# Optimization experiments

Measured on AMD Instinct MI355X. Metric: run time of the kernel, lower is better.

The kernel has to match this reference:

```python
import jax, jax.numpy as jnp
import numpy as np

B, T, I, H, OUT, L = 256, 1200, 16, 128, 1, 2


def _lstm_layer(x, W_ih, W_hh, b_ih, b_hh):
    # x: [B, T, Din]; W_ih: [4H, Din]; W_hh: [4H, H]
    # Precompute input contribution for all timesteps (one big GEMM),
    # then scan only the recurrent part.
    pre = jnp.einsum('btd,gd->btg', x, W_ih) + b_ih + b_hh  # [B, T, 4H]
    pre = jnp.swapaxes(pre, 0, 1)  # [T, B, 4H]
    h0 = jnp.zeros((x.shape[0], W_hh.shape[1]), dtype=x.dtype)
    c0 = jnp.zeros_like(h0)

    def step(carry, p_t):
        h, c = carry
        g = p_t + h @ W_hh.T  # [B, 4H]
        i, f, gg, o = jnp.split(g, 4, axis=-1)  # torch gate order: i, f, g, o
        i = jax.nn.sigmoid(i)
        f = jax.nn.sigmoid(f)
        gg = jnp.tanh(gg)
        o = jax.nn.sigmoid(o)
        c = f * c + i * gg
        h = o * jnp.tanh(c)
        return (h, c), h

    (_, _), hs = jax.lax.scan(step, (h0, c0), pre)  # hs: [T, B, H]
    return jnp.swapaxes(hs, 0, 1)  # [B, T, H]


def setup_inputs() -> dict:
    key = jax.random.key(0)
    ks = jax.random.split(key, 12)
    s = 0.08  # small init scale to keep gates unsaturated
    inp = {
        'x': jax.random.normal(ks[0], (B, T, I), dtype=jnp.float32),
        'W_ih0': jax.random.normal(ks[1], (4 * H, I), dtype=jnp.float32) * s,
        'W_hh0': jax.random.normal(ks[2], (4 * H, H), dtype=jnp.float32) * s,
        'b_ih0': jax.random.normal(ks[3], (4 * H,), dtype=jnp.float32) * s,
        'b_hh0': jax.random.normal(ks[4], (4 * H,), dtype=jnp.float32) * s,
        'W_ih1': jax.random.normal(ks[5], (4 * H, H), dtype=jnp.float32) * s,
        'W_hh1': jax.random.normal(ks[6], (4 * H, H), dtype=jnp.float32) * s,
        'b_ih1': jax.random.normal(ks[7], (4 * H,), dtype=jnp.float32) * s,
        'b_hh1': jax.random.normal(ks[8], (4 * H,), dtype=jnp.float32) * s,
        'W_lin': jax.random.normal(ks[9], (OUT, H), dtype=jnp.float32) * s,
        'b_lin': jax.random.normal(ks[10], (OUT,), dtype=jnp.float32) * s,
    }
    return inp


def reference(x, W_ih0, W_hh0, b_ih0, b_hh0, W_ih1, W_hh1, b_ih1, b_hh1, W_lin, b_lin):
    h1 = _lstm_layer(x, W_ih0, W_hh0, b_ih0, b_hh0)   # [B, T, H]
    h2 = _lstm_layer(h1, W_ih1, W_hh1, b_ih1, b_hh1)  # [B, T, H]
    out = jax.nn.relu(h2)
    out = jnp.einsum('bth,oh->bto', out, W_lin) + b_lin  # [B, T, OUT]
    return out.reshape(-1, 12)  # [B*T*OUT/12, 12]
```

## Files before the change

kernel.cpp:

```cpp
#include <hip/hip_runtime.h>
#include <hip/hip_fp16.h>

#define B_ 256
#define T_ 1200
#define I_ 16
#define H_ 128

typedef __attribute__((ext_vector_type(2))) _Float16 h2;
typedef __attribute__((ext_vector_type(8))) _Float16 f16x8;

union f16x8u { f16x8 v; h2 h[4]; _Float16 s[8]; };

#if __has_builtin(__builtin_amdgcn_fdot2)
__device__ __forceinline__ float fdot2(h2 a, h2 b, float c) {
  return __builtin_amdgcn_fdot2(a, b, c, false);
}
#else
__device__ __forceinline__ float fdot2(h2 a, h2 b, float c) {
  return fmaf((float)a.x, (float)b.x, fmaf((float)a.y, (float)b.y, c));
}
#endif

template <int PAT>
__device__ __forceinline__ float qbcast(float x) {
  return __int_as_float(__builtin_amdgcn_update_dpp(0, __float_as_int(x), PAT, 0xF, 0xF, true));
}

__device__ __forceinline__ float wred(float x) {
  x += __int_as_float(__builtin_amdgcn_update_dpp(0, __float_as_int(x), 0x141, 0xF, 0xF, true));
  x += __int_as_float(__builtin_amdgcn_update_dpp(0, __float_as_int(x), 0x140, 0xF, 0xF, true));
  x += __shfl_xor(x, 16);
  x += __shfl_xor(x, 32);
  return x;
}

__device__ __forceinline__ float tanh_(float x) {
  return 1.f - 2.f * __builtin_amdgcn_rcpf(1.f + __expf(2.f * x));
}

__device__ __forceinline__ void load_row_h2(const float* __restrict__ p, h2* w) {
#pragma unroll
  for (int i = 0; i < 32; ++i) {
    const float4 v = *(const float4*)(p + 4 * i);
    w[2 * i].x     = (_Float16)v.x; w[2 * i].y     = (_Float16)v.y;
    w[2 * i + 1].x = (_Float16)v.z; w[2 * i + 1].y = (_Float16)v.w;
  }
}

__device__ __forceinline__ void lds_barrier() {
  __builtin_amdgcn_sched_barrier(0);
  asm volatile("s_waitcnt lgkmcnt(0)" ::: "memory");
  __builtin_amdgcn_s_barrier();
  __builtin_amdgcn_sched_barrier(0);
}

__global__ __launch_bounds__(512, 2) void lstm_one(
    const float* __restrict__ xin,
    const float* __restrict__ Wih0, const float* __restrict__ Whh0,
    const float* __restrict__ bih0, const float* __restrict__ bhh0,
    const float* __restrict__ Wih1, const float* __restrict__ Whh1,
    const float* __restrict__ bih1, const float* __restrict__ bhh1,
    const float* __restrict__ Wlin, const float* __restrict__ blin,
    float* __restrict__ out)
{
  __shared__ __align__(16) __half xs[T_ * I_];
  __shared__ __align__(16) __half h0b[2][H_];
  __shared__ __align__(16) __half h1b[2][H_];
  __shared__ __align__(16) float red[2][8];

  const int tid = threadIdx.x;
  const int q = tid & 3;
  const int j = tid >> 2;
  const int g = q * H_ + j;
  const int b = blockIdx.x;

  {
    const float4* xg4 = (const float4*)(xin + (size_t)b * T_ * I_);
    for (int idx = tid; idx < T_ * I_ / 4; idx += 512) {
      const float4 v = xg4[idx];
      xs[4 * idx]     = __float2half(v.x);
      xs[4 * idx + 1] = __float2half(v.y);
      xs[4 * idx + 2] = __float2half(v.z);
      xs[4 * idx + 3] = __float2half(v.w);
    }
  }

  h2 w0[64], wi[64], w1[64], wx[8];
  load_row_h2(Whh0 + (size_t)g * H_, w0);
  load_row_h2(Wih1 + (size_t)g * H_, wi);
  load_row_h2(Whh1 + (size_t)g * H_, w1);
  {
    const float* px = Wih0 + (size_t)g * I_;
#pragma unroll
    for (int i = 0; i < 4; ++i) {
      const float4 v = *(const float4*)(px + 4 * i);
      wx[2 * i].x     = (_Float16)v.x; wx[2 * i].y     = (_Float16)v.y;
      wx[2 * i + 1].x = (_Float16)v.z; wx[2 * i + 1].y = (_Float16)v.w;
    }
  }
  const float bs0 = bih0[g] + bhh0[g];
  const float bs1 = bih1[g] + bhh1[g];
  const float wl = Wlin[j];
  const float bl = blin[0];
  const float s0 = (q == 2) ? 1.f : 0.f;
  const float s1 = (q == 2) ? -2.f : 1.f;
  const float s2 = (q == 2) ? 2.f : -1.f;

  if (tid < H_) {
    h0b[0][tid] = __float2half(0.f);
    h1b[0][tid] = __float2half(0.f);
    h1b[1][tid] = __float2half(0.f);
  }
  float cst0 = 0.f, cst1 = 0.f, hv1p = 0.f;
  float* op = out + (size_t)b * T_;
  __syncthreads();

#pragma unroll 1
  for (int u = 0; u <= T_ + 2; ++u) {
    const int rb = u & 1, nb = rb ^ 1;

    if (u >= 2 && u <= T_ + 1) {
      const float val = wred(fmaxf(hv1p, 0.f) * wl);
      if ((tid & 63) == 0) red[rb][tid >> 6] = val;
    }
    if (u >= 3) {
      const int m = u - 3;
      if (tid == ((m & 7) << 6)) {
        const float4 r0 = *(const float4*)(&red[nb][0]);
        const float4 r1 = *(const float4*)(&red[nb][4]);
        op[m] = bl + r0.x + r0.y + r0.z + r0.w + r1.x + r1.y + r1.z + r1.w;
      }
    }

    float A0 = 0.f, A1 = 0.f, A2 = 0.f, A3 = 0.f;
    float B0 = 0.f, B1 = 0.f, B2 = 0.f, B3 = 0.f;
    float C0 = 0.f, C1 = 0.f, C2 = 0.f, C3 = 0.f;

    if (u >= 1 && u < T_) {
#pragma unroll
      for (int i = 0; i < 16; ++i) {
        f16x8u u8; u8.v = *(const f16x8*)(&h0b[rb][8 * i]);
        A0 = fdot2(w0[4 * i],     u8.h[0], A0);
        A1 = fdot2(w0[4 * i + 1], u8.h[1], A1);
        A2 = fdot2(w0[4 * i + 2], u8.h[2], A2);
        A3 = fdot2(w0[4 * i + 3], u8.h[3], A3);
        B0 = fdot2(wi[4 * i],     u8.h[0], B0);
        B1 = fdot2(wi[4 * i + 1], u8.h[1], B1);
        B2 = fdot2(wi[4 * i + 2], u8.h[2], B2);
        B3 = fdot2(wi[4 * i + 3], u8.h[3], B3);
      }
    } else if (u == T_) {
#pragma unroll
      for (int i = 0; i < 16; ++i) {
        f16x8u u8; u8.v = *(const f16x8*)(&h0b[rb][8 * i]);
        B0 = fdot2(wi[4 * i],     u8.h[0], B0);
        B1 = fdot2(wi[4 * i + 1], u8.h[1], B1);
        B2 = fdot2(wi[4 * i + 2], u8.h[2], B2);
        B3 = fdot2(wi[4 * i + 3], u8.h[3], B3);
      }
    }

    if (u < T_) {
#pragma unroll
      for (int m2 = 0; m2 < 2; ++m2) {
        f16x8u u8; u8.v = *(const f16x8*)(&xs[u * I_ + 8 * m2]);
        A0 = fdot2(wx[4 * m2],     u8.h[0], A0);
        A1 = fdot2(wx[4 * m2 + 1], u8.h[1], A1);
        A2 = fdot2(wx[4 * m2 + 2], u8.h[2], A2);
        A3 = fdot2(wx[4 * m2 + 3], u8.h[3], A3);
      }
      const float pre = (A0 + A1) + (A2 + A3) + bs0;
      const float act = fmaf(s1, __builtin_amdgcn_rcpf(1.f + __expf(s2 * pre)), s0);
      const float ig = qbcast<0x00>(act);
      const float fg = qbcast<0x55>(act);
      const float gg = qbcast<0xAA>(act);
      const float og = qbcast<0xFF>(act);
      cst0 = fg * cst0 + ig * gg;
      const float hv0 = og * tanh_(cst0);
      if (q == 0) h0b[nb][j] = __float2half(hv0);
    }

    if (u >= 1 && u <= T_) {
#pragma unroll
      for (int i = 0; i < 16; ++i) {
        f16x8u u8; u8.v = *(const f16x8*)(&h1b[rb][8 * i]);
        C0 = fdot2(w1[4 * i],     u8.h[0], C0);
        C1 = fdot2(w1[4 * i + 1], u8.h[1], C1);
        C2 = fdot2(w1[4 * i + 2], u8.h[2], C2);
        C3 = fdot2(w1[4 * i + 3], u8.h[3], C3);
      }
      const float pre = (B0 + B1) + (B2 + B3) + (C0 + C1) + (C2 + C3) + bs1;
      const float act = fmaf(s1, __builtin_amdgcn_rcpf(1.f + __expf(s2 * pre)), s0);
      const float ig = qbcast<0x00>(act);
      const float fg = qbcast<0x55>(act);
      const float gg = qbcast<0xAA>(act);
      const float og = qbcast<0xFF>(act);
      cst1 = fg * cst1 + ig * gg;
      hv1p = og * tanh_(cst1);
      if (q == 0) h1b[nb][j] = __float2half(hv1p);
    }

    if (u <= T_ + 1) lds_barrier();
  }
}

extern "C" void kernel_launch(void* const* d_in, const int* in_sizes, int n_in,
                              void* d_out, int out_size, void* d_ws, size_t ws_size,
                              hipStream_t stream) {
  lstm_one<<<B_, 512, 0, stream>>>(
      (const float*)d_in[0],
      (const float*)d_in[1], (const float*)d_in[2],
      (const float*)d_in[3], (const float*)d_in[4],
      (const float*)d_in[5], (const float*)d_in[6],
      (const float*)d_in[7], (const float*)d_in[8],
      (const float*)d_in[9], (const float*)d_in[10],
      (float*)d_out);
}
```

Baseline: 1.933 ms.

## Split each LSTM unit's dot products across 8 lanes with DPP reductions

The block grows from 512 to 1024 threads. Each group of 8 lanes now owns one hidden unit and computes all four gates, with each lane covering a 16-element slice of the hidden vector; partial sums are combined by DPP adds. This shortens the serial fdot2 chain per thread and cuts the weight registers held by each lane, aiming at lower per-timestep latency in this latency-bound recurrence. In exchange it adds cross-lane reduction steps, makes every lane compute the activations redundantly, moves the biases into LDS, and runs the dot-product loops unconditionally on every step.

Measured after the change: 2.836 ms. 1.47x slower.

```diff
diff --git a/kernel.cpp b/kernel.cpp
--- a/kernel.cpp
+++ b/kernel.cpp
@@ -21,30 +21,30 @@
 }
 #endif
 
-template <int PAT>
-__device__ __forceinline__ float qbcast(float x) {
-  return __int_as_float(__builtin_amdgcn_update_dpp(0, __float_as_int(x), PAT, 0xF, 0xF, true));
-}
-
-__device__ __forceinline__ float wred(float x) {
-  x += __int_as_float(__builtin_amdgcn_update_dpp(0, __float_as_int(x), 0x141, 0xF, 0xF, true));
-  x += __int_as_float(__builtin_amdgcn_update_dpp(0, __float_as_int(x), 0x140, 0xF, 0xF, true));
+template <int CTRL>
+__device__ __forceinline__ float dppadd(float x) {
+  return x + __int_as_float(__builtin_amdgcn_update_dpp(0, __float_as_int(x), CTRL, 0xF, 0xF, true));
+}
+
+__device__ __forceinline__ float qsum8(float x) {
+  x = dppadd<0xB1>(x);
+  x = dppadd<0x4E>(x);
+  x = dppadd<0x141>(x);
+  return x;
+}
+
+__device__ __forceinline__ float ored(float x) {
+  x = dppadd<0x140>(x);
   x += __shfl_xor(x, 16);
   x += __shfl_xor(x, 32);
   return x;
 }
 
+__device__ __forceinline__ float sigm(float x) {
+  return __builtin_amdgcn_rcpf(1.f + __expf(-x));
+}
 __device__ __forceinline__ float tanh_(float x) {
   return 1.f - 2.f * __builtin_amdgcn_rcpf(1.f + __expf(2.f * x));
-}
-
-__device__ __forceinline__ void load_row_h2(const float* __restrict__ p, h2* w) {
-#pragma unroll
-  for (int i = 0; i < 32; ++i) {
-    const float4 v = *(const float4*)(p + 4 * i);
-    w[2 * i].x     = (_Float16)v.x; w[2 * i].y     = (_Float16)v.y;
-    w[2 * i + 1].x = (_Float16)v.z; w[2 * i + 1].y = (_Float16)v.w;
-  }
 }
 
 __device__ __forceinline__ void lds_barrier() {
@@ -54,7 +54,7 @@
   __builtin_amdgcn_sched_barrier(0);
 }
 
-__global__ __launch_bounds__(512, 2) void lstm_one(
+__global__ __launch_bounds__(1024, 4) void lstm_oct(
     const float* __restrict__ xin,
     const float* __restrict__ Wih0, const float* __restrict__ Whh0,
     const float* __restrict__ bih0, const float* __restrict__ bhh0,
@@ -66,17 +66,17 @@
   __shared__ __align__(16) __half xs[T_ * I_];
   __shared__ __align__(16) __half h0b[2][H_];
   __shared__ __align__(16) __half h1b[2][H_];
-  __shared__ __align__(16) float red[2][8];
+  __shared__ __align__(16) float lbs[H_][8];
+  __shared__ __align__(16) float red[2][16];
 
   const int tid = threadIdx.x;
-  const int q = tid & 3;
-  const int j = tid >> 2;
-  const int g = q * H_ + j;
+  const int c = tid & 7;
+  const int j = tid >> 3;
   const int b = blockIdx.x;
 
   {
     const float4* xg4 = (const float4*)(xin + (size_t)b * T_ * I_);
-    for (int idx = tid; idx < T_ * I_ / 4; idx += 512) {
+    for (int idx = tid; idx < T_ * I_ / 4; idx += 1024) {
       const float4 v = xg4[idx];
       xs[4 * idx]     = __float2half(v.x);
       xs[4 * idx + 1] = __float2half(v.y);
@@ -85,32 +85,42 @@
     }
   }
 
-  h2 w0[64], wi[64], w1[64], wx[8];
-  load_row_h2(Whh0 + (size_t)g * H_, w0);
-  load_row_h2(Wih1 + (size_t)g * H_, wi);
-  load_row_h2(Whh1 + (size_t)g * H_, w1);
-  {
-    const float* px = Wih0 + (size_t)g * I_;
+  h2 wA[4][8], wI[4][8], wH[4][8], wx[4];
+#pragma unroll
+  for (int q = 0; q < 4; ++q) {
+    const int g = q * H_ + j;
+    const float* pA = Whh0 + (size_t)g * H_ + c * 16;
+    const float* pI = Wih1 + (size_t)g * H_ + c * 16;
+    const float* pH = Whh1 + (size_t)g * H_ + c * 16;
 #pragma unroll
     for (int i = 0; i < 4; ++i) {
-      const float4 v = *(const float4*)(px + 4 * i);
-      wx[2 * i].x     = (_Float16)v.x; wx[2 * i].y     = (_Float16)v.y;
-      wx[2 * i + 1].x = (_Float16)v.z; wx[2 * i + 1].y = (_Float16)v.w;
-    }
-  }
-  const float bs0 = bih0[g] + bhh0[g];
-  const float bs1 = bih1[g] + bhh1[g];
-  const float wl = Wlin[j];
-  const float bl = blin[0];
-  const float s0 = (q == 2) ? 1.f : 0.f;
-  const float s1 = (q == 2) ? -2.f : 1.f;
-  const float s2 = (q == 2) ? 2.f : -1.f;
+      float4 v = *(const float4*)(pA + 4 * i);
+      wA[q][2*i].x   = (_Float16)v.x; wA[q][2*i].y   = (_Float16)v.y;
+      wA[q][2*i+1].x = (_Float16)v.z; wA[q][2*i+1].y = (_Float16)v.w;
+      v = *(const float4*)(pI + 4 * i);
+      wI[q][2*i].x   = (_Float16)v.x; wI[q][2*i].y   = (_Float16)v.y;
+      wI[q][2*i+1].x = (_Float16)v.z; wI[q][2*i+1].y = (_Float16)v.w;
+      v = *(const float4*)(pH + 4 * i);
+      wH[q][2*i].x   = (_Float16)v.x; wH[q][2*i].y   = (_Float16)v.y;
+      wH[q][2*i+1].x = (_Float16)v.z; wH[q][2*i+1].y = (_Float16)v.w;
+    }
+    const float2 vx = *(const float2*)(Wih0 + (size_t)g * I_ + 2 * c);
+    wx[q].x = (_Float16)vx.x; wx[q].y = (_Float16)vx.y;
+  }
 
   if (tid < H_) {
+#pragma unroll
+    for (int q = 0; q < 4; ++q) {
+      lbs[tid][q]     = bih0[q * H_ + tid] + bhh0[q * H_ + tid];
+      lbs[tid][4 + q] = bih1[q * H_ + tid] + bhh1[q * H_ + tid];
+    }
     h0b[0][tid] = __float2half(0.f);
     h1b[0][tid] = __float2half(0.f);
     h1b[1][tid] = __float2half(0.f);
   }
+  const float wl = Wlin[j];
+  const float bl = blin[0];
+
   float cst0 = 0.f, cst1 = 0.f, hv1p = 0.f;
   float* op = out + (size_t)b * T_;
   __syncthreads();
@@ -120,94 +130,117 @@
     const int rb = u & 1, nb = rb ^ 1;
 
     if (u >= 2 && u <= T_ + 1) {
-      const float val = wred(fmaxf(hv1p, 0.f) * wl);
+      const float val = ored(fmaxf(hv1p, 0.f) * wl);
       if ((tid & 63) == 0) red[rb][tid >> 6] = val;
     }
     if (u >= 3) {
       const int m = u - 3;
-      if (tid == ((m & 7) << 6)) {
+      if (tid == ((m & 15) << 6)) {
         const float4 r0 = *(const float4*)(&red[nb][0]);
         const float4 r1 = *(const float4*)(&red[nb][4]);
-        op[m] = bl + r0.x + r0.y + r0.z + r0.w + r1.x + r1.y + r1.z + r1.w;
-      }
-    }
-
+        const float4 r2 = *(const float4*)(&red[nb][8]);
+        const float4 r3 = *(const float4*)(&red[nb][12]);
+        op[m] = bl
+            + r0.x + r0.y + r0.z + r0.w + r1.x + r1.y + r1.z + r1.w
+            + r2.x + r2.y + r2.z + r2.w + r3.x + r3.y + r3.z + r3.w;
+      }
+    }
+
+    const float4 bs0v = *(const float4*)(&lbs[j][0]);
+    const float4 bs1v = *(const float4*)(&lbs[j][4]);
+
+    const int xi = (u < T_) ? u : 0;
+    const h2 xv = *(const h2*)(&xs[xi * I_ + 2 * c]);
     float A0 = 0.f, A1 = 0.f, A2 = 0.f, A3 = 0.f;
-    float B0 = 0.f, B1 = 0.f, B2 = 0.f, B3 = 0.f;
-    float C0 = 0.f, C1 = 0.f, C2 = 0.f, C3 = 0.f;
-
-    if (u >= 1 && u < T_) {
-#pragma unroll
-      for (int i = 0; i < 16; ++i) {
-        f16x8u u8; u8.v = *(const f16x8*)(&h0b[rb][8 * i]);
-        A0 = fdot2(w0[4 * i],     u8.h[0], A0);
-        A1 = fdot2(w0[4 * i + 1], u8.h[1], A1);
-        A2 = fdot2(w0[4 * i + 2], u8.h[2], A2);
-        A3 = fdot2(w0[4 * i + 3], u8.h[3], A3);
-        B0 = fdot2(wi[4 * i],     u8.h[0], B0);
-        B1 = fdot2(wi[4 * i + 1], u8.h[1], B1);
-        B2 = fdot2(wi[4 * i + 2], u8.h[2], B2);
-        B3 = fdot2(wi[4 * i + 3], u8.h[3], B3);
-      }
-    } else if (u == T_) {
-#pragma unroll
-      for (int i = 0; i < 16; ++i) {
-        f16x8u u8; u8.v = *(const f16x8*)(&h0b[rb][8 * i]);
-        B0 = fdot2(wi[4 * i],     u8.h[0], B0);
-        B1 = fdot2(wi[4 * i + 1], u8.h[1], B1);
-        B2 = fdot2(wi[4 * i + 2], u8.h[2], B2);
-        B3 = fdot2(wi[4 * i + 3], u8.h[3], B3);
-      }
-    }
-
+    {
+      f16x8u ua, ub;
+      ua.v = *(const f16x8*)(&h0b[rb][c * 16]);
+      ub.v = *(const f16x8*)(&h0b[rb][c * 16 + 8]);
+#pragma unroll
+      for (int k = 0; k < 4; ++k) {
+        A0 = fdot2(wA[0][k], ua.h[k], A0);
+        A1 = fdot2(wA[1][k], ua.h[k], A1);
+        A2 = fdot2(wA[2][k], ua.h[k], A2);
+        A3 = fdot2(wA[3][k], ua.h[k], A3);
+      }
+#pragma unroll
+      for (int k = 0; k < 4; ++k) {
+        A0 = fdot2(wA[0][4 + k], ub.h[k], A0);
+        A1 = fdot2(wA[1][4 + k], ub.h[k], A1);
+        A2 = fdot2(wA[2][4 + k], ub.h[k], A2);
+        A3 = fdot2(wA[3][4 + k], ub.h[k], A3);
+      }
+    }
+    A0 = fdot2(wx[0], xv, A0);
+    A1 = fdot2(wx[1], xv, A1);
+    A2 = fdot2(wx[2], xv, A2);
+    A3 = fdot2(wx[3], xv, A3);
     if (u < T_) {
-#pragma unroll
-      for (int m2 = 0; m2 < 2; ++m2) {
-        f16x8u u8; u8.v = *(const f16x8*)(&xs[u * I_ + 8 * m2]);
-        A0 = fdot2(wx[4 * m2],     u8.h[0], A0);
-        A1 = fdot2(wx[4 * m2 + 1], u8.h[1], A1);
-        A2 = fdot2(wx[4 * m2 + 2], u8.h[2], A2);
-        A3 = fdot2(wx[4 * m2 + 3], u8.h[3], A3);
-      }
-      const float pre = (A0 + A1) + (A2 + A3) + bs0;
-      const float act = fmaf(s1, __builtin_amdgcn_rcpf(1.f + __expf(s2 * pre)), s0);
-      const float ig = qbcast<0x00>(act);
-      const float fg = qbcast<0x55>(act);
-      const float gg = qbcast<0xAA>(act);
-      const float og = qbcast<0xFF>(act);
+      const float g0 = qsum8(A0) + bs0v.x;
+      const float g1 = qsum8(A1) + bs0v.y;
+      const float g2 = qsum8(A2) + bs0v.z;
+      const float g3 = qsum8(A3) + bs0v.w;
+      const float ig = sigm(g0), fg = sigm(g1), gg = tanh_(g2), og = sigm(g3);
       cst0 = fg * cst0 + ig * gg;
       const float hv0 = og * tanh_(cst0);
-      if (q == 0) h0b[nb][j] = __float2half(hv0);
-    }
-
+      if (c == 0) h0b[nb][j] = __float2half(hv0);
+    }
+
+    float C0 = 0.f, C1 = 0.f, C2 = 0.f, C3 = 0.f;
+    {
+      f16x8u ua, ub, va, vb;
+      ua.v = *(const f16x8*)(&h0b[rb][c * 16]);
+      ub.v = *(const f16x8*)(&h0b[rb][c * 16 + 8]);
+      va.v = *(const f16x8*)(&h1b[rb][c * 16]);
+      vb.v = *(const f16x8*)(&h1b[rb][c * 16 + 8]);
+#pragma unroll
+      for (int k = 0; k < 4; ++k) {
+        C0 = fdot2(wI[0][k], ua.h[k], C0);
+        C1 = fdot2(wI[1][k], ua.h[k], C1);
+        C2 = fdot2(wI[2][k], ua.h[k], C2);
+        C3 = fdot2(wI[3][k], ua.h[k], C3);
+      }
+#pragma unroll
+      for (int k = 0; k < 4; ++k) {
+        C0 = fdot2(wI[0][4 + k], ub.h[k], C0);
+        C1 = fdot2(wI[1][4 + k], ub.h[k], C1);
+        C2 = fdot2(wI[2][4 + k], ub.h[k], C2);
+        C3 = fdot2(wI[3][4 + k], ub.h[k], C3);
+      }
+#pragma unroll
+      for (int k = 0; k < 4; ++k) {
+        C0 = fdot2(wH[0][k], va.h[k], C0);
+        C1 = fdot2(wH[1][k], va.h[k], C1);
+        C2 = fdot2(wH[2][k], va.h[k], C2);
+        C3 = fdot2(wH[3][k], va.h[k], C3);
+      }
+#pragma unroll
+      for (int k = 0; k < 4; ++k) {
+        C0 = fdot2(wH[0][4 + k], vb.h[k], C0);
+        C1 = fdot2(wH[1][4 + k], vb.h[k], C1);
+        C2 = fdot2(wH[2][4 + k], vb.h[k], C2);
+        C3 = fdot2(wH[3][4 + k], vb.h[k], C3);
+      }
+    }
     if (u >= 1 && u <= T_) {
-#pragma unroll
-      for (int i = 0; i < 16; ++i) {
-        f16x8u u8; u8.v = *(const f16x8*)(&h1b[rb][8 * i]);
-        C0 = fdot2(w1[4 * i],     u8.h[0], C0);
-        C1 = fdot2(w1[4 * i + 1], u8.h[1], C1);
-        C2 = fdot2(w1[4 * i + 2], u8.h[2], C2);
-        C3 = fdot2(w1[4 * i + 3], u8.h[3], C3);
-      }
-      const float pre = (B0 + B1) + (B2 + B3) + (C0 + C1) + (C2 + C3) + bs1;
-      const float act = fmaf(s1, __builtin_amdgcn_rcpf(1.f + __expf(s2 * pre)), s0);
-      const float ig = qbcast<0x00>(act);
-      const float fg = qbcast<0x55>(act);
-      const float gg = qbcast<0xAA>(act);
-      const float og = qbcast<0xFF>(act);
+      const float g0 = qsum8(C0) + bs1v.x;
+      const float g1 = qsum8(C1) + bs1v.y;
+      const float g2 = qsum8(C2) + bs1v.z;
+      const float g3 = qsum8(C3) + bs1v.w;
+      const float ig = sigm(g0), fg = sigm(g1), gg = tanh_(g2), og = sigm(g3);
       cst1 = fg * cst1 + ig * gg;
       hv1p = og * tanh_(cst1);
-      if (q == 0) h1b[nb][j] = __float2half(hv1p);
-    }
-
-    if (u <= T_ + 1) lds_barrier();
+      if (c == 0) h1b[nb][j] = __float2half(hv1p);
+    }
+
+    lds_barrier();
   }
 }
 
 extern "C" void kernel_launch(void* const* d_in, const int* in_sizes, int n_in,
                               void* d_out, int out_size, void* d_ws, size_t ws_size,
                               hipStream_t stream) {
-  lstm_one<<<B_, 512, 0, stream>>>(
+  lstm_oct<<<B_, 1024, 0, stream>>>(
       (const float*)d_in[0],
       (const float*)d_in[1], (const float*)d_in[2],
       (const float*)d_in[3], (const float*)d_in[4],
```
